# Performance work log

Measured on AMD Instinct MI355X. Metric: run time of the kernel, lower is better.

The kernel has to match this reference:

```python
import jax, jax.numpy as jnp
import numpy as np

N_NODES = 50000
N_EDGES = 600000
N_GRAPHS = 1024
H = 128
VOCAB = 32
NC = 2
BN_EPS = 1e-5


def setup_inputs() -> dict:
    key = jax.random.key(0)
    ks = jax.random.split(key, 16)
    rn = lambda k, s, sc=0.05: jax.random.normal(k, s, jnp.float32) * sc
    inp = {}
    inp["node_feat"] = jax.random.randint(ks[0], (N_NODES,), 0, VOCAB, dtype=jnp.int32)
    inp["edge_src"] = jax.random.randint(ks[1], (N_EDGES,), 0, N_NODES, dtype=jnp.int32)
    inp["edge_dst"] = jax.random.randint(ks[2], (N_EDGES,), 0, N_NODES, dtype=jnp.int32)
    inp["graph_ids"] = jnp.sort(jax.random.randint(ks[3], (N_NODES,), 0, N_GRAPHS, dtype=jnp.int32))
    inp["emb"] = rn(ks[4], (VOCAB, H))
    inp["W1"] = rn(ks[5], (H, H)); inp["b1"] = jnp.zeros((H,), jnp.float32)
    inp["W2"] = rn(ks[6], (H, H)); inp["b2"] = jnp.zeros((H,), jnp.float32)
    inp["e1_w"] = rn(ks[7], (H, H));   inp["e1_b"] = jnp.zeros((H,), jnp.float32)
    inp["e2_w"] = rn(ks[8], (H, H));   inp["e2_b"] = jnp.zeros((H,), jnp.float32)
    inp["e3_w"] = rn(ks[9], (H, 64));  inp["e3_b"] = jnp.zeros((64,), jnp.float32)
    inp["e4_w"] = rn(ks[10], (64, 32)); inp["e4_b"] = jnp.zeros((32,), jnp.float32)
    inp["e5_w"] = rn(ks[11], (32, NC)); inp["e5_b"] = jnp.zeros((NC,), jnp.float32)
    inp["bn0_g"] = jnp.ones((H,), jnp.float32); inp["bn0_b"] = jnp.zeros((H,), jnp.float32)
    inp["bn1_g"] = jnp.ones((H,), jnp.float32); inp["bn1_b"] = jnp.zeros((H,), jnp.float32)
    return inp


def reference(node_feat, edge_src, edge_dst, graph_ids,
              emb, W1, b1, W2, b2,
              e1_w, e1_b, e2_w, e2_b, e3_w, e3_b, e4_w, e4_b, e5_w, e5_b,
              bn0_g, bn0_b, bn1_g, bn1_b):
    ones_e = jnp.ones((N_EDGES,), jnp.float32)
    out_deg = jax.ops.segment_sum(ones_e, edge_src, num_segments=N_NODES)
    in_deg = jax.ops.segment_sum(ones_e, edge_dst, num_segments=N_NODES)
    # DGL GraphConv norm='both': D_out^{-1/2} pre-scale, D_in^{-1/2} post-scale (deg clamped to 1)
    oi = jax.lax.rsqrt(jnp.maximum(out_deg, 1.0))  # [N]
    ii = jax.lax.rsqrt(jnp.maximum(in_deg, 1.0))   # [N]

    def gconv(h, W, b):
        m = (h * oi[:, None])[edge_src]                                   # [E,H] gather
        agg = jax.ops.segment_sum(m, edge_dst, num_segments=N_NODES)      # [N,H] scatter-add
        return (agg * ii[:, None]) @ W + b

    h = emb[node_feat]                       # [N,H] embedding lookup
    h = jax.nn.relu(gconv(h, W1, b1))
    h = jax.nn.relu(gconv(h, W2, b2))

    # dgl.mean_nodes: per-graph mean over nodes
    cnt = jax.ops.segment_sum(jnp.ones((N_NODES,), jnp.float32), graph_ids, num_segments=N_GRAPHS)
    hg = jax.ops.segment_sum(h, graph_ids, num_segments=N_GRAPHS) / jnp.maximum(cnt, 1.0)[:, None]

    def bn(x, g, b):  # BatchNorm1d, training-mode batch stats (biased var)
        mu = x.mean(0)
        var = x.var(0)
        return (x - mu) * jax.lax.rsqrt(var + BN_EPS) * g + b

    def lrelu(x, s):
        return jnp.where(x >= 0, x, s * x)

    h1 = lrelu(bn(hg @ e1_w + e1_b, bn0_g, bn0_b), 0.05)
    h2 = lrelu(bn(h1 @ e2_w + e2_b, bn1_g, bn1_b), 0.05)
    h3 = lrelu(h2 @ e3_w + e3_b, 0.1)
    h4 = lrelu(h3 @ e4_w + e4_b, 0.1)
    y = h4 @ e5_w + e5_b                      # [G, NC]
    return jax.nn.log_softmax(y, axis=1)
```

## Files before the change

### kernel.cpp

```cpp
#include <hip/hip_runtime.h>
#include <hip/hip_bf16.h>
#include <math.h>

#define N_NODES 50000
#define N_PAD   50048
#define N_EDGES 600000
#define N_GRAPHS 1024
#define H 128
#define VOCAB 32
#define BN_EPS 1e-5f
#define SCAN_BLOCKS ((N_NODES + 255) / 256)
#define H1_NODES 64

typedef short bf8_t __attribute__((ext_vector_type(8)));
typedef float f4_t __attribute__((ext_vector_type(4)));


__global__ void k_countO(const int* __restrict__ src, int* __restrict__ cntO, int E) {
    int i = blockIdx.x * blockDim.x + threadIdx.x;
    if (i < E) atomicAdd(&cntO[src[i]], 1);
}

__global__ void k_oi(const int* __restrict__ cntO, float* __restrict__ oi, int n) {
    int i = blockIdx.x * blockDim.x + threadIdx.x;
    if (i < n) oi[i] = rsqrtf(fmaxf((float)cntO[i], 1.f));
}

__global__ void k_hist64(const int* __restrict__ src, const int* __restrict__ dst,
                         const int* __restrict__ feat, const float* __restrict__ oi,
                         unsigned long long* __restrict__ wc,
                         unsigned char* __restrict__ rank8, int E) {
    int i = blockIdx.x * blockDim.x + threadIdx.x;
    if (i >= E) return;
    int s = src[i], d = dst[i], v = feat[s];
    unsigned long long q = (unsigned long long)__float2uint_rn(oi[s] * 16777216.0f);
    unsigned long long old = atomicAdd(&wc[(size_t)d * VOCAB + v], (1ULL << 40) | q);
    rank8[i] = (unsigned char)(old >> 40);
}

__global__ void k_nodebins(const unsigned long long* __restrict__ wc,
                           int* __restrict__ cntI, unsigned char* __restrict__ binbase,
                           int n) {
    int wid = threadIdx.x >> 6;
    int lane = threadIdx.x & 63;
    int node = blockIdx.x * 4 + wid;
    if (node >= n || lane >= VOCAB) return;
    int c = (int)(wc[(size_t)node * VOCAB + lane] >> 40);
    int inc = c;
#pragma unroll
    for (int off = 1; off < VOCAB; off <<= 1) {
        int u = __shfl_up(inc, off, 64);
        if (lane >= off) inc += u;
    }
    binbase[(size_t)node * VOCAB + lane] = (unsigned char)(inc - c);
    if (lane == VOCAB - 1) cntI[node] = inc;
}

__global__ void k_fill2(const int* __restrict__ src, const int* __restrict__ dst,
                        const int* __restrict__ feat, const int* __restrict__ row_ptr,
                        const unsigned char* __restrict__ binbase,
                        const unsigned char* __restrict__ rank8,
                        int* __restrict__ col, int E) {
    int i = blockIdx.x * blockDim.x + threadIdx.x;
    if (i >= E) return;
    int s = src[i], d = dst[i], v = feat[s];
    int slot = row_ptr[d] + (int)binbase[(size_t)d * VOCAB + v] + (int)rank8[i];
    col[slot] = s;
}


__global__ void k_blocksum(const int* __restrict__ cnt, int* __restrict__ bsum, int n) {
    __shared__ int red[256];
    int i = blockIdx.x * 256 + threadIdx.x;
    red[threadIdx.x] = (i < n) ? cnt[i] : 0;
    __syncthreads();
    for (int off = 128; off > 0; off >>= 1) {
        if (threadIdx.x < off) red[threadIdx.x] += red[threadIdx.x + off];
        __syncthreads();
    }
    if (threadIdx.x == 0) bsum[blockIdx.x] = red[0];
}

__global__ void k_scanbsum(int* __restrict__ bsum, int* __restrict__ row_ptr_last, int nb) {
    __shared__ int sh[256];
    int t = threadIdx.x;
    int v = (t < nb) ? bsum[t] : 0;
    sh[t] = v;
    __syncthreads();
    for (int off = 1; off < 256; off <<= 1) {
        int u = (t >= off) ? sh[t - off] : 0;
        __syncthreads();
        sh[t] += u;
        __syncthreads();
    }
    if (t < nb) bsum[t] = sh[t] - v;
    if (t == nb - 1) *row_ptr_last = sh[t];
}

__global__ void k_scatterscan(const int* __restrict__ cntI, const int* __restrict__ bsum,
                              int* __restrict__ row_ptr, float* __restrict__ ii, int n) {
    __shared__ int sh[256];
    int i = blockIdx.x * 256 + threadIdx.x;
    int t = threadIdx.x;
    int v = (i < n) ? cntI[i] : 0;
    sh[t] = v;
    __syncthreads();
    for (int off = 1; off < 256; off <<= 1) {
        int u = (t >= off) ? sh[t - off] : 0;
        __syncthreads();
        sh[t] += u;
        __syncthreads();
    }
    if (i < n) {
        row_ptr[i] = bsum[blockIdx.x] + sh[t] - v;
        ii[i] = rsqrtf(fmaxf((float)v, 1.f));
    }
}


__global__ void k_emb1(const float* __restrict__ emb, const float* __restrict__ W1,
                       float* __restrict__ emb1) {
    int v = blockIdx.x;
    int j = threadIdx.x;
    float acc = 0.f;
    for (int k = 0; k < H; ++k) acc += emb[v * H + k] * W1[k * H + j];
    emb1[v * H + j] = acc;
}

__global__ void k_w2t(const float* __restrict__ W, __hip_bfloat16* __restrict__ WT) {
    int k = blockIdx.x;
    int c = threadIdx.x;
    WT[(size_t)c * H + k] = __float2bfloat16(W[(size_t)k * H + c]);
}

__global__ void k_h1(const unsigned long long* __restrict__ wc, const float* __restrict__ emb1,
                     const float* __restrict__ ii, const float* __restrict__ oi,
                     const float* __restrict__ b1, __hip_bfloat16* __restrict__ h1, int n) {
    __shared__ float wl[H1_NODES * VOCAB];
    __shared__ float sii[H1_NODES], soi[H1_NODES];
    int tid = threadIdx.x;
    int j = tid & 127;
    int g = tid >> 7;
    float ev[VOCAB];
#pragma unroll
    for (int v = 0; v < VOCAB; ++v) ev[v] = emb1[v * H + j];
    float bj = b1[j];

    int node0 = blockIdx.x * H1_NODES;
    int nn = min(H1_NODES, n - node0);
    const unsigned long long* wsrc = wc + (size_t)node0 * VOCAB;
    for (int i = tid; i < nn * VOCAB; i += 256) {
        unsigned long long p = wsrc[i];
        float lo = (float)((unsigned)p & 0xFFFFFFu);
        float hi = (float)((unsigned)(p >> 24) & 0xFFFFu);
        wl[i] = fmaf(lo, 1.0f / 16777216.0f, hi);
    }
    for (int i = tid; i < nn; i += 256) { sii[i] = ii[node0 + i]; soi[i] = oi[node0 + i]; }
    __syncthreads();

    int rbeg = g * 32;
    int rend = min(rbeg + 32, nn);
    for (int r = rbeg; r < rend; ++r) {
        const float4* wr = (const float4*)(wl + r * VOCAB);
        float acc = 0.f;
#pragma unroll
        for (int q = 0; q < VOCAB / 4; ++q) {
            float4 w4 = wr[q];
            acc += w4.x * ev[4 * q] + w4.y * ev[4 * q + 1]
                 + w4.z * ev[4 * q + 2] + w4.w * ev[4 * q + 3];
        }
        float val = fmaxf(acc * sii[r] + bj, 0.f);
        h1[(size_t)(node0 + r) * H + j] = __float2bfloat16(val * soi[r]);
    }
}


__global__ void k_gather_bf(const __hip_bfloat16* __restrict__ h,
                            const int* __restrict__ row_ptr, const int* __restrict__ col,
                            __hip_bfloat16* __restrict__ out, int n) {
    int gid = blockIdx.x * blockDim.x + threadIdx.x;
    int node = gid >> 6;
    int lane = gid & 63;
    if (node >= n) return;
    int beg = row_ptr[node];
    int end = row_ptr[node + 1];
    int lo = lane * 2;
    float a0 = 0.f, a1 = 0.f;
    int e = beg;
    for (; e + 8 <= end; e += 8) {
#pragma unroll
        for (int k = 0; k < 8; ++k) {
            int s = col[e + k];
            float2 f = __bfloat1622float2(*(const __hip_bfloat162*)(h + (size_t)s * H + lo));
            a0 += f.x; a1 += f.y;
        }
    }
    for (; e < end; ++e) {
        int s = col[e];
        float2 f = __bfloat1622float2(*(const __hip_bfloat162*)(h + (size_t)s * H + lo));
        a0 += f.x; a1 += f.y;
    }
    *(__hip_bfloat162*)(out + (size_t)node * H + lo) =
        __float22bfloat162_rn(make_float2(a0, a1));
}

__global__ void k_transform_mfma(const __hip_bfloat16* __restrict__ A,
                                 const __hip_bfloat16* __restrict__ WT,
                                 const float* __restrict__ ii,
                                 const float* __restrict__ b,
                                 float* __restrict__ outp, int n) {
    int wave = threadIdx.x >> 6;
    int lane = threadIdx.x & 63;
    int row0 = blockIdx.x * 64 + wave * 16;
    int rl = lane & 15;
    int kg = lane >> 4;
    f4_t acc[8];
#pragma unroll
    for (int t = 0; t < 8; ++t) acc[t] = f4_t{0.f, 0.f, 0.f, 0.f};
    const __hip_bfloat16* arow = A + (size_t)(row0 + rl) * H + kg * 8;
#pragma unroll
    for (int ks = 0; ks < 4; ++ks) {
        bf8_t a = *(const bf8_t*)(arow + ks * 32);
#pragma unroll
        for (int t = 0; t < 8; ++t) {
            bf8_t bf = *(const bf8_t*)(WT + (size_t)(t * 16 + rl) * H + ks * 32 + kg * 8);
            acc[t] = __builtin_amdgcn_mfma_f32_16x16x32_bf16(a, bf, acc[t], 0, 0, 0);
        }
    }
    int rbase = row0 + kg * 4;
#pragma unroll
    for (int r = 0; r < 4; ++r) {
        int node = rbase + r;
        if (node < n) {
            float s = ii[node];
#pragma unroll
            for (int t = 0; t < 8; ++t) {
                int c = t * 16 + rl;
                float v = acc[t][r] * s + b[c];
                outp[(size_t)node * H + c] = fmaxf(v, 0.f);
            }
        }
    }
}

__global__ void k_pool(const float* __restrict__ h, const int* __restrict__ gid,
                       float* __restrict__ hg, int n) {
    int g = blockIdx.x;
    __shared__ int sh[2];
    if (threadIdx.x == 0) {
        int lo = 0, hi = n;
        while (lo < hi) { int m = (lo + hi) >> 1; if (gid[m] < g) lo = m + 1; else hi = m; }
        sh[0] = lo;
        int lo2 = lo, hi2 = n;
        while (lo2 < hi2) { int m = (lo2 + hi2) >> 1; if (gid[m] < g + 1) lo2 = m + 1; else hi2 = m; }
        sh[1] = lo2;
    }
    __syncthreads();
    int beg = sh[0], end = sh[1];
    int c = threadIdx.x;
    float s = 0.f;
    for (int i = beg; i < end; ++i) s += h[(size_t)i * H + c];
    float cnt = (float)(end - beg);
    hg[g * H + c] = s / fmaxf(cnt, 1.f);
}


__global__ void k_mlp1(const float* __restrict__ in, const float* __restrict__ W,
                       const float* __restrict__ b, float* __restrict__ out) {
    __shared__ float ld[128];
    int g = blockIdx.x;
    int t = threadIdx.x;
    ld[t] = in[g * H + t];
    __syncthreads();
    float acc = b[t];
    for (int k = 0; k < H; ++k) acc += ld[k] * W[k * H + t];
    out[g * H + t] = acc;
}

__global__ void k_bnstat(const float* __restrict__ x, float* __restrict__ stats, int G) {
    int c = blockIdx.x;
    float s = 0.f, s2 = 0.f;
    for (int g = threadIdx.x; g < G; g += blockDim.x) {
        float v = x[g * H + c];
        s += v; s2 += v * v;
    }
    __shared__ float rs[256], rs2[256];
    rs[threadIdx.x] = s; rs2[threadIdx.x] = s2;
    __syncthreads();
    for (int off = 128; off > 0; off >>= 1) {
        if (threadIdx.x < off) { rs[threadIdx.x] += rs[threadIdx.x + off]; rs2[threadIdx.x] += rs2[threadIdx.x + off]; }
        __syncthreads();
    }
    if (threadIdx.x == 0) {
        float mu = rs[0] / G;
        stats[c] = mu;
        stats[H + c] = rs2[0] / G - mu * mu;
    }
}

__global__ void k_mlp2bn(const float* __restrict__ t1, const float* __restrict__ stats,
                         const float* __restrict__ gam, const float* __restrict__ bet,
                         const float* __restrict__ W, const float* __restrict__ bias,
                         float* __restrict__ t2) {
    __shared__ float x[128];
    int g = blockIdx.x, t = threadIdx.x;
    float v = t1[g * H + t];
    v = (v - stats[t]) * rsqrtf(stats[H + t] + BN_EPS) * gam[t] + bet[t];
    x[t] = (v >= 0.f) ? v : 0.05f * v;
    __syncthreads();
    float acc = bias[t];
    for (int k = 0; k < H; ++k) acc += x[k] * W[k * H + t];
    t2[g * H + t] = acc;
}

__global__ void k_head(const float* __restrict__ t2, const float* __restrict__ stats,
                       const float* __restrict__ gam, const float* __restrict__ bet,
                       const float* __restrict__ e3w, const float* __restrict__ e3b,
                       const float* __restrict__ e4w, const float* __restrict__ e4b,
                       const float* __restrict__ e5w, const float* __restrict__ e5b,
                       float* __restrict__ out) {
    __shared__ float x[128], h3[64], h4[32];
    int g = blockIdx.x, t = threadIdx.x;
    float v = t2[g * H + t];
    v = (v - stats[t]) * rsqrtf(stats[H + t] + BN_EPS) * gam[t] + bet[t];
    x[t] = (v >= 0.f) ? v : 0.05f * v;
    __syncthreads();
    if (t < 64) {
        float a = e3b[t];
        for (int k = 0; k < 128; ++k) a += x[k] * e3w[k * 64 + t];
        h3[t] = (a >= 0.f) ? a : 0.1f * a;
    }
    __syncthreads();
    if (t < 32) {
        float a = e4b[t];
        for (int k = 0; k < 64; ++k) a += h3[k] * e4w[k * 32 + t];
        h4[t] = (a >= 0.f) ? a : 0.1f * a;
    }
    __syncthreads();
    if (t == 0) {
        float y0 = e5b[0], y1 = e5b[1];
        for (int k = 0; k < 32; ++k) {
            y0 += h4[k] * e5w[2 * k];
            y1 += h4[k] * e5w[2 * k + 1];
        }
        float m = fmaxf(y0, y1);
        float l = m + logf(expf(y0 - m) + expf(y1 - m));
        out[2 * g] = y0 - l;
        out[2 * g + 1] = y1 - l;
    }
}

extern "C" void kernel_launch(void* const* d_in, const int* in_sizes, int n_in,
                              void* d_out, int out_size, void* d_ws, size_t ws_size,
                              hipStream_t stream) {
    const int*   node_feat = (const int*)d_in[0];
    const int*   edge_src  = (const int*)d_in[1];
    const int*   edge_dst  = (const int*)d_in[2];
    const int*   graph_ids = (const int*)d_in[3];
    const float* emb  = (const float*)d_in[4];
    const float* W1   = (const float*)d_in[5];
    const float* b1   = (const float*)d_in[6];
    const float* W2   = (const float*)d_in[7];
    const float* b2   = (const float*)d_in[8];
    const float* e1_w = (const float*)d_in[9];
    const float* e1_b = (const float*)d_in[10];
    const float* e2_w = (const float*)d_in[11];
    const float* e2_b = (const float*)d_in[12];
    const float* e3_w = (const float*)d_in[13];
    const float* e3_b = (const float*)d_in[14];
    const float* e4_w = (const float*)d_in[15];
    const float* e4_b = (const float*)d_in[16];
    const float* e5_w = (const float*)d_in[17];
    const float* e5_b = (const float*)d_in[18];
    const float* bn0_g = (const float*)d_in[19];
    const float* bn0_b = (const float*)d_in[20];
    const float* bn1_g = (const float*)d_in[21];
    const float* bn1_b = (const float*)d_in[22];
    float* out = (float*)d_out;

    float* ws = (float*)d_ws;
    float* bufA = ws;
    __hip_bfloat16* h1bf = (__hip_bfloat16*)(bufA + (size_t)N_NODES * H);
    __hip_bfloat16* aggbf = h1bf + (size_t)N_NODES * H;
    int*   cntO = (int*)(aggbf + (size_t)N_PAD * H);
    unsigned long long* wc = (unsigned long long*)(cntO + N_NODES);
    float* oi   = (float*)(wc + (size_t)N_NODES * VOCAB);
    float* ii   = oi + N_NODES;
    int*   cntI = (int*)(ii + N_NODES);
    int*   row_ptr = cntI + N_NODES;
    int*   col  = row_ptr + 50048;
    unsigned char* binbase = (unsigned char*)(col + N_EDGES);
    unsigned char* rank8   = binbase + (size_t)N_NODES * VOCAB;
    float* hg   = (float*)(rank8 + ((N_EDGES + 63) & ~63));
    float* t1   = hg + N_GRAPHS * H;
    float* t2   = t1 + N_GRAPHS * H;
    float* stats = t2 + N_GRAPHS * H;
    int*   bsum  = (int*)(stats + 4 * H);
    float* emb1  = (float*)(bsum + 256);
    __hip_bfloat16* w2t = (__hip_bfloat16*)(emb1 + VOCAB * H);

    hipMemsetAsync(cntO, 0, N_NODES * sizeof(int) + (size_t)N_NODES * VOCAB * 8, stream);

    const int eb = (N_EDGES + 255) / 256;
    k_countO<<<eb, 256, 0, stream>>>(edge_src, cntO, N_EDGES);
    k_oi<<<SCAN_BLOCKS, 256, 0, stream>>>(cntO, oi, N_NODES);
    k_emb1<<<VOCAB, 128, 0, stream>>>(emb, W1, emb1);
    k_w2t<<<H, 128, 0, stream>>>(W2, w2t);
    k_hist64<<<eb, 256, 0, stream>>>(edge_src, edge_dst, node_feat, oi, wc, rank8, N_EDGES);
    k_nodebins<<<(N_NODES + 3) / 4, 256, 0, stream>>>(wc, cntI, binbase, N_NODES);
    k_blocksum<<<SCAN_BLOCKS, 256, 0, stream>>>(cntI, bsum, N_NODES);
    k_scanbsum<<<1, 256, 0, stream>>>(bsum, row_ptr + N_NODES, SCAN_BLOCKS);
    k_scatterscan<<<SCAN_BLOCKS, 256, 0, stream>>>(cntI, bsum, row_ptr, ii, N_NODES);
    k_fill2<<<eb, 256, 0, stream>>>(edge_src, edge_dst, node_feat, row_ptr, binbase, rank8, col, N_EDGES);

    k_h1<<<(N_NODES + H1_NODES - 1) / H1_NODES, 256, 0, stream>>>(wc, emb1, ii, oi, b1, h1bf, N_NODES);

    const int gb = (N_NODES * 64 + 255) / 256;
    k_gather_bf<<<gb, 256, 0, stream>>>(h1bf, row_ptr, col, aggbf, N_NODES);
    k_transform_mfma<<<(N_NODES + 63) / 64, 256, 0, stream>>>(aggbf, w2t, ii, b2, bufA, N_NODES);

    k_pool<<<N_GRAPHS, 128, 0, stream>>>(bufA, graph_ids, hg, N_NODES);

    k_mlp1<<<N_GRAPHS, 128, 0, stream>>>(hg, e1_w, e1_b, t1);
    k_bnstat<<<H, 256, 0, stream>>>(t1, stats, N_GRAPHS);
    k_mlp2bn<<<N_GRAPHS, 128, 0, stream>>>(t1, stats, bn0_g, bn0_b, e2_w, e2_b, t2);
    k_bnstat<<<H, 256, 0, stream>>>(t2, stats + 2 * H, N_GRAPHS);
    k_head<<<N_GRAPHS, 128, 0, stream>>>(t2, stats + 2 * H, bn1_g, bn1_b,
                                         e3_w, e3_b, e4_w, e4_b, e5_w, e5_b, out);
}
```

Baseline: 230.3 us.

## Fuse preprocessing kernels and widen gather to two nodes per wave

Merges several small launches: degree counting is combined with the emb@W1 and W2-transpose prep, the oi computation is inlined where it is used, the block sum moves into the node-bin kernel, the CSR fill shares a launch with the h1 computation, and pooling is fused with the first MLP layer. The gather kernel now assigns half a wave per node with 4-element bf16 loads, doubling the number of nodes each wave handles. The goal is to cut launch overhead and intermediate buffers. The cost is that rsqrt is recomputed per edge, and the fill and h1 blocks now run in one launch, which is valid only because h1 does not read col.

```diff
diff --git a/kernel.cpp b/kernel.cpp
--- a/kernel.cpp
+++ b/kernel.cpp
@@ -11,74 +11,85 @@
 #define BN_EPS 1e-5f
 #define SCAN_BLOCKS ((N_NODES + 255) / 256)
 #define H1_NODES 64
+#define EB ((N_EDGES + 255) / 256)
 
 typedef short bf8_t __attribute__((ext_vector_type(8)));
 typedef float f4_t __attribute__((ext_vector_type(4)));
 
-
-__global__ void k_countO(const int* __restrict__ src, int* __restrict__ cntO, int E) {
-    int i = blockIdx.x * blockDim.x + threadIdx.x;
-    if (i < E) atomicAdd(&cntO[src[i]], 1);
-}
-
-__global__ void k_oi(const int* __restrict__ cntO, float* __restrict__ oi, int n) {
-    int i = blockIdx.x * blockDim.x + threadIdx.x;
-    if (i < n) oi[i] = rsqrtf(fmaxf((float)cntO[i], 1.f));
+__global__ void k_count_prep(const int* __restrict__ src, int* __restrict__ cntO,
+                             const float* __restrict__ emb, const float* __restrict__ W1,
+                             float* __restrict__ emb1,
+                             const float* __restrict__ W2, __hip_bfloat16* __restrict__ w2t) {
+    int b = blockIdx.x;
+    int t = threadIdx.x;
+    if (b < EB) {
+        int i = b * 256 + t;
+        if (i < N_EDGES) atomicAdd(&cntO[src[i]], 1);
+    } else if (b < EB + 32) {
+        if (t < 128) {
+            int v = b - EB;
+            float acc = 0.f;
+            for (int k = 0; k < H; ++k) acc += emb[v * H + k] * W1[k * H + t];
+            emb1[v * H + t] = acc;
+        }
+    } else {
+        if (t < 128) {
+            int k = b - EB - 32;
+            w2t[(size_t)t * H + k] = __float2bfloat16(W2[(size_t)k * H + t]);
+        }
+    }
 }
 
 __global__ void k_hist64(const int* __restrict__ src, const int* __restrict__ dst,
-                         const int* __restrict__ feat, const float* __restrict__ oi,
+                         const int* __restrict__ feat, const int* __restrict__ cntO,
                          unsigned long long* __restrict__ wc,
                          unsigned char* __restrict__ rank8, int E) {
     int i = blockIdx.x * blockDim.x + threadIdx.x;
     if (i >= E) return;
     int s = src[i], d = dst[i], v = feat[s];
-    unsigned long long q = (unsigned long long)__float2uint_rn(oi[s] * 16777216.0f);
+    float o = rsqrtf(fmaxf((float)cntO[s], 1.f));
+    unsigned long long q = (unsigned long long)__float2uint_rn(o * 16777216.0f);
     unsigned long long old = atomicAdd(&wc[(size_t)d * VOCAB + v], (1ULL << 40) | q);
     rank8[i] = (unsigned char)(old >> 40);
 }
 
 __global__ void k_nodebins(const unsigned long long* __restrict__ wc,
                            int* __restrict__ cntI, unsigned char* __restrict__ binbase,
-                           int n) {
-    int wid = threadIdx.x >> 6;
-    int lane = threadIdx.x & 63;
-    int node = blockIdx.x * 4 + wid;
-    if (node >= n || lane >= VOCAB) return;
-    int c = (int)(wc[(size_t)node * VOCAB + lane] >> 40);
-    int inc = c;
-#pragma unroll
-    for (int off = 1; off < VOCAB; off <<= 1) {
-        int u = __shfl_up(inc, off, 64);
-        if (lane >= off) inc += u;
-    }
-    binbase[(size_t)node * VOCAB + lane] = (unsigned char)(inc - c);
-    if (lane == VOCAB - 1) cntI[node] = inc;
-}
-
-__global__ void k_fill2(const int* __restrict__ src, const int* __restrict__ dst,
-                        const int* __restrict__ feat, const int* __restrict__ row_ptr,
-                        const unsigned char* __restrict__ binbase,
-                        const unsigned char* __restrict__ rank8,
-                        int* __restrict__ col, int E) {
-    int i = blockIdx.x * blockDim.x + threadIdx.x;
-    if (i >= E) return;
-    int s = src[i], d = dst[i], v = feat[s];
-    int slot = row_ptr[d] + (int)binbase[(size_t)d * VOCAB + v] + (int)rank8[i];
-    col[slot] = s;
-}
-
-
-__global__ void k_blocksum(const int* __restrict__ cnt, int* __restrict__ bsum, int n) {
+                           int* __restrict__ bsum, int n) {
+    __shared__ int scnt[256];
+    int t = threadIdx.x;
+    int wave = t >> 6, lane = t & 63;
+    int sub = lane >> 5;
+    int l32 = lane & 31;
+    int nodeBase = blockIdx.x * 256;
+#pragma unroll 4
+    for (int it = 0; it < 32; ++it) {
+        int local = wave * 64 + it * 2 + sub;
+        int node = nodeBase + local;
+        int c = 0;
+        if (node < n && l32 < VOCAB)
+            c = (int)(wc[(size_t)node * VOCAB + l32] >> 40);
+        int inc = c;
+#pragma unroll
+        for (int off = 1; off < VOCAB; off <<= 1) {
+            int u = __shfl_up(inc, off, 32);
+            if (l32 >= off) inc += u;
+        }
+        if (node < n && l32 < VOCAB)
+            binbase[(size_t)node * VOCAB + l32] = (unsigned char)(inc - c);
+        if (l32 == VOCAB - 1) scnt[local] = (node < n) ? inc : 0;
+    }
+    __syncthreads();
+    int node = nodeBase + t;
+    if (node < n) cntI[node] = scnt[t];
     __shared__ int red[256];
-    int i = blockIdx.x * 256 + threadIdx.x;
-    red[threadIdx.x] = (i < n) ? cnt[i] : 0;
+    red[t] = scnt[t];
     __syncthreads();
     for (int off = 128; off > 0; off >>= 1) {
-        if (threadIdx.x < off) red[threadIdx.x] += red[threadIdx.x + off];
-        __syncthreads();
-    }
-    if (threadIdx.x == 0) bsum[blockIdx.x] = red[0];
+        if (t < off) red[t] += red[t + off];
+        __syncthreads();
+    }
+    if (t == 0) bsum[blockIdx.x] = red[0];
 }
 
 __global__ void k_scanbsum(int* __restrict__ bsum, int* __restrict__ row_ptr_last, int nb) {
@@ -117,28 +128,29 @@
     }
 }
 
-
-__global__ void k_emb1(const float* __restrict__ emb, const float* __restrict__ W1,
-                       float* __restrict__ emb1) {
-    int v = blockIdx.x;
-    int j = threadIdx.x;
-    float acc = 0.f;
-    for (int k = 0; k < H; ++k) acc += emb[v * H + k] * W1[k * H + j];
-    emb1[v * H + j] = acc;
-}
-
-__global__ void k_w2t(const float* __restrict__ W, __hip_bfloat16* __restrict__ WT) {
-    int k = blockIdx.x;
-    int c = threadIdx.x;
-    WT[(size_t)c * H + k] = __float2bfloat16(W[(size_t)k * H + c]);
-}
-
-__global__ void k_h1(const unsigned long long* __restrict__ wc, const float* __restrict__ emb1,
-                     const float* __restrict__ ii, const float* __restrict__ oi,
-                     const float* __restrict__ b1, __hip_bfloat16* __restrict__ h1, int n) {
+#define H1_BLOCKS ((N_NODES + H1_NODES - 1) / H1_NODES)
+__global__ void k_fill_h1(const int* __restrict__ src, const int* __restrict__ dst,
+                          const int* __restrict__ feat, const int* __restrict__ row_ptr,
+                          const unsigned char* __restrict__ binbase,
+                          const unsigned char* __restrict__ rank8,
+                          int* __restrict__ col,
+                          const unsigned long long* __restrict__ wc,
+                          const float* __restrict__ emb1,
+                          const float* __restrict__ ii, const int* __restrict__ cntO,
+                          const float* __restrict__ b1, __hip_bfloat16* __restrict__ h1) {
     __shared__ float wl[H1_NODES * VOCAB];
     __shared__ float sii[H1_NODES], soi[H1_NODES];
     int tid = threadIdx.x;
+    if (blockIdx.x < EB) {
+        int i = blockIdx.x * 256 + tid;
+        if (i < N_EDGES) {
+            int s = src[i], d = dst[i], v = feat[s];
+            int slot = row_ptr[d] + (int)binbase[(size_t)d * VOCAB + v] + (int)rank8[i];
+            col[slot] = s;
+        }
+        return;
+    }
+    int hb = blockIdx.x - EB;
     int j = tid & 127;
     int g = tid >> 7;
     float ev[VOCAB];
@@ -146,8 +158,8 @@
     for (int v = 0; v < VOCAB; ++v) ev[v] = emb1[v * H + j];
     float bj = b1[j];
 
-    int node0 = blockIdx.x * H1_NODES;
-    int nn = min(H1_NODES, n - node0);
+    int node0 = hb * H1_NODES;
+    int nn = min(H1_NODES, N_NODES - node0);
     const unsigned long long* wsrc = wc + (size_t)node0 * VOCAB;
     for (int i = tid; i < nn * VOCAB; i += 256) {
         unsigned long long p = wsrc[i];
@@ -155,7 +167,10 @@
         float hi = (float)((unsigned)(p >> 24) & 0xFFFFu);
         wl[i] = fmaf(lo, 1.0f / 16777216.0f, hi);
     }
-    for (int i = tid; i < nn; i += 256) { sii[i] = ii[node0 + i]; soi[i] = oi[node0 + i]; }
+    for (int i = tid; i < nn; i += 256) {
+        sii[i] = ii[node0 + i];
+        soi[i] = rsqrtf(fmaxf((float)cntO[node0 + i], 1.f));
+    }
     __syncthreads();
 
     int rbeg = g * 32;
@@ -174,34 +189,43 @@
     }
 }
 
-
 __global__ void k_gather_bf(const __hip_bfloat16* __restrict__ h,
                             const int* __restrict__ row_ptr, const int* __restrict__ col,
                             __hip_bfloat16* __restrict__ out, int n) {
     int gid = blockIdx.x * blockDim.x + threadIdx.x;
-    int node = gid >> 6;
+    int wid = gid >> 6;
     int lane = gid & 63;
+    int node = wid * 2 + (lane >> 5);
+    int l32 = lane & 31;
     if (node >= n) return;
     int beg = row_ptr[node];
     int end = row_ptr[node + 1];
-    int lo = lane * 2;
-    float a0 = 0.f, a1 = 0.f;
+    int co = l32 * 4;
+    float a0 = 0.f, a1 = 0.f, a2 = 0.f, a3 = 0.f;
     int e = beg;
     for (; e + 8 <= end; e += 8) {
 #pragma unroll
         for (int k = 0; k < 8; ++k) {
             int s = col[e + k];
-            float2 f = __bfloat1622float2(*(const __hip_bfloat162*)(h + (size_t)s * H + lo));
-            a0 += f.x; a1 += f.y;
+            uint2 v = *(const uint2*)(h + (size_t)s * H + co);
+            float2 f0 = __bfloat1622float2(*(__hip_bfloat162*)&v.x);
+            float2 f1 = __bfloat1622float2(*(__hip_bfloat162*)&v.y);
+            a0 += f0.x; a1 += f0.y; a2 += f1.x; a3 += f1.y;
         }
     }
     for (; e < end; ++e) {
         int s = col[e];
-        float2 f = __bfloat1622float2(*(const __hip_bfloat162*)(h + (size_t)s * H + lo));
-        a0 += f.x; a1 += f.y;
-    }
-    *(__hip_bfloat162*)(out + (size_t)node * H + lo) =
-        __float22bfloat162_rn(make_float2(a0, a1));
+        uint2 v = *(const uint2*)(h + (size_t)s * H + co);
+        float2 f0 = __bfloat1622float2(*(__hip_bfloat162*)&v.x);
+        float2 f1 = __bfloat1622float2(*(__hip_bfloat162*)&v.y);
+        a0 += f0.x; a1 += f0.y; a2 += f1.x; a3 += f1.y;
+    }
+    __hip_bfloat162 o0 = __float22bfloat162_rn(make_float2(a0, a1));
+    __hip_bfloat162 o1 = __float22bfloat162_rn(make_float2(a2, a3));
+    uint2 ov;
+    ov.x = *(unsigned*)&o0;
+    ov.y = *(unsigned*)&o1;
+    *(uint2*)(out + (size_t)node * H + co) = ov;
 }
 
 __global__ void k_transform_mfma(const __hip_bfloat16* __restrict__ A,
@@ -243,38 +267,29 @@
     }
 }
 
-__global__ void k_pool(const float* __restrict__ h, const int* __restrict__ gid,
-                       float* __restrict__ hg, int n) {
-    int g = blockIdx.x;
-    __shared__ int sh[2];
-    if (threadIdx.x == 0) {
+__global__ void k_poolmlp1(const float* __restrict__ h, const int* __restrict__ gid,
+                           const float* __restrict__ e1w, const float* __restrict__ e1b,
+                           float* __restrict__ t1, int n) {
+    __shared__ int bnd[2];
+    __shared__ float row[128];
+    int g = blockIdx.x, t = threadIdx.x;
+    if (t == 0) {
         int lo = 0, hi = n;
         while (lo < hi) { int m = (lo + hi) >> 1; if (gid[m] < g) lo = m + 1; else hi = m; }
-        sh[0] = lo;
+        bnd[0] = lo;
         int lo2 = lo, hi2 = n;
         while (lo2 < hi2) { int m = (lo2 + hi2) >> 1; if (gid[m] < g + 1) lo2 = m + 1; else hi2 = m; }
-        sh[1] = lo2;
-    }
-    __syncthreads();
-    int beg = sh[0], end = sh[1];
-    int c = threadIdx.x;
+        bnd[1] = lo2;
+    }
+    __syncthreads();
+    int beg = bnd[0], end = bnd[1];
     float s = 0.f;
-    for (int i = beg; i < end; ++i) s += h[(size_t)i * H + c];
-    float cnt = (float)(end - beg);
-    hg[g * H + c] = s / fmaxf(cnt, 1.f);
-}
-
-
-__global__ void k_mlp1(const float* __restrict__ in, const float* __restrict__ W,
-                       const float* __restrict__ b, float* __restrict__ out) {
-    __shared__ float ld[128];
-    int g = blockIdx.x;
-    int t = threadIdx.x;
-    ld[t] = in[g * H + t];
-    __syncthreads();
-    float acc = b[t];
-    for (int k = 0; k < H; ++k) acc += ld[k] * W[k * H + t];
-    out[g * H + t] = acc;
+    for (int i = beg; i < end; ++i) s += h[(size_t)i * H + t];
+    row[t] = s / fmaxf((float)(end - beg), 1.f);
+    __syncthreads();
+    float acc = e1b[t];
+    for (int k = 0; k < H; ++k) acc += row[k] * e1w[k * H + t];
+    t1[g * H + t] = acc;
 }
 
 __global__ void k_bnstat(const float* __restrict__ x, float* __restrict__ stats, int G) {
@@ -384,15 +399,13 @@
     __hip_bfloat16* aggbf = h1bf + (size_t)N_NODES * H;
     int*   cntO = (int*)(aggbf + (size_t)N_PAD * H);
     unsigned long long* wc = (unsigned long long*)(cntO + N_NODES);
-    float* oi   = (float*)(wc + (size_t)N_NODES * VOCAB);
-    float* ii   = oi + N_NODES;
+    float* ii   = (float*)(wc + (size_t)N_NODES * VOCAB);
     int*   cntI = (int*)(ii + N_NODES);
     int*   row_ptr = cntI + N_NODES;
     int*   col  = row_ptr + 50048;
     unsigned char* binbase = (unsigned char*)(col + N_EDGES);
     unsigned char* rank8   = binbase + (size_t)N_NODES * VOCAB;
-    float* hg   = (float*)(rank8 + ((N_EDGES + 63) & ~63));
-    float* t1   = hg + N_GRAPHS * H;
+    float* t1   = (float*)(rank8 + ((N_EDGES + 63) & ~63));
     float* t2   = t1 + N_GRAPHS * H;
     float* stats = t2 + N_GRAPHS * H;
     int*   bsum  = (int*)(stats + 4 * H);
@@ -401,27 +414,20 @@
 
     hipMemsetAsync(cntO, 0, N_NODES * sizeof(int) + (size_t)N_NODES * VOCAB * 8, stream);
 
-    const int eb = (N_EDGES + 255) / 256;
-    k_countO<<<eb, 256, 0, stream>>>(edge_src, cntO, N_EDGES);
-    k_oi<<<SCAN_BLOCKS, 256, 0, stream>>>(cntO, oi, N_NODES);
-    k_emb1<<<VOCAB, 128, 0, stream>>>(emb, W1, emb1);
-    k_w2t<<<H, 128, 0, stream>>>(W2, w2t);
-    k_hist64<<<eb, 256, 0, stream>>>(edge_src, edge_dst, node_feat, oi, wc, rank8, N_EDGES);
-    k_nodebins<<<(N_NODES + 3) / 4, 256, 0, stream>>>(wc, cntI, binbase, N_NODES);
-    k_blocksum<<<SCAN_BLOCKS, 256, 0, stream>>>(cntI, bsum, N_NODES);
+    k_count_prep<<<EB + 160, 256, 0, stream>>>(edge_src, cntO, emb, W1, emb1, W2, w2t);
+    k_hist64<<<EB, 256, 0, stream>>>(edge_src, edge_dst, node_feat, cntO, wc, rank8, N_EDGES);
+    k_nodebins<<<SCAN_BLOCKS, 256, 0, stream>>>(wc, cntI, binbase, bsum, N_NODES);
     k_scanbsum<<<1, 256, 0, stream>>>(bsum, row_ptr + N_NODES, SCAN_BLOCKS);
     k_scatterscan<<<SCAN_BLOCKS, 256, 0, stream>>>(cntI, bsum, row_ptr, ii, N_NODES);
-    k_fill2<<<eb, 256, 0, stream>>>(edge_src, edge_dst, node_feat, row_ptr, binbase, rank8, col, N_EDGES);
-
-    k_h1<<<(N_NODES + H1_NODES - 1) / H1_NODES, 256, 0, stream>>>(wc, emb1, ii, oi, b1, h1bf, N_NODES);
-
-    const int gb = (N_NODES * 64 + 255) / 256;
+    k_fill_h1<<<EB + H1_BLOCKS, 256, 0, stream>>>(edge_src, edge_dst, node_feat, row_ptr,
+                                                  binbase, rank8, col,
+                                                  wc, emb1, ii, cntO, b1, h1bf);
+
+    const int gb = ((N_NODES + 1) / 2 * 64 + 255) / 256;
     k_gather_bf<<<gb, 256, 0, stream>>>(h1bf, row_ptr, col, aggbf, N_NODES);
     k_transform_mfma<<<(N_NODES + 63) / 64, 256, 0, stream>>>(aggbf, w2t, ii, b2, bufA, N_NODES);
 
-    k_pool<<<N_GRAPHS, 128, 0, stream>>>(bufA, graph_ids, hg, N_NODES);
-
-    k_mlp1<<<N_GRAPHS, 128, 0, stream>>>(hg, e1_w, e1_b, t1);
+    k_poolmlp1<<<N_GRAPHS, 128, 0, stream>>>(bufA, graph_ids, e1_w, e1_b, t1, N_NODES);
     k_bnstat<<<H, 256, 0, stream>>>(t1, stats, N_GRAPHS);
     k_mlp2bn<<<N_GRAPHS, 128, 0, stream>>>(t1, stats, bn0_g, bn0_b, e2_w, e2_b, t2);
     k_bnstat<<<H, 256, 0, stream>>>(t2, stats + 2 * H, N_GRAPHS);
```

New measurement: 220.6 us. -4.2%, faster.
